# Kernel optimization log

Hardware: AMD Instinct MI355X
Metric: run time of the kernel (lower is better)

Reference implementation:

```python
import jax, jax.numpy as jnp
import numpy as np

NUM_GRAPHS = 64

def setup_inputs() -> dict:
    key = jax.random.key(0)
    ks = jax.random.split(key, 10)
    N, E, D, V = 100000, 1600000, 64, 30
    node_types = jax.random.randint(ks[0], (N,), 0, V, dtype=jnp.int64 if jax.config.jax_enable_x64 else jnp.int32)
    edge_index = jax.random.randint(ks[1], (2, E), 0, N, dtype=jnp.int32)
    batch = jnp.sort(jax.random.randint(ks[2], (N,), 0, NUM_GRAPHS, dtype=jnp.int32))
    emb_table = jax.random.normal(ks[3], (V, D), dtype=jnp.float32)
    W1 = jax.random.normal(ks[4], (D, D), dtype=jnp.float32) / np.sqrt(D)
    W2 = jax.random.normal(ks[5], (D, D), dtype=jnp.float32) / np.sqrt(D)
    W3 = jax.random.normal(ks[6], (D, D), dtype=jnp.float32) / np.sqrt(D)
    b1 = jnp.zeros((D,), jnp.float32)
    b2 = jnp.zeros((D,), jnp.float32)
    b3 = jnp.zeros((D,), jnp.float32)
    return {"node_types": node_types, "edge_index": edge_index, "batch": batch,
            "emb_table": emb_table, "W1": W1, "b1": b1, "W2": W2, "b2": b2, "W3": W3, "b3": b3}

def _gcn_conv(x, W, b, row, col, norm, N):
    # x' = D^-1/2 (A+I) D^-1/2 (x @ W) + b   (PyG GCNConv semantics)
    h = x @ W
    msg = h[row] * norm[:, None]              # gather + edgewise scale
    out = jax.ops.segment_sum(msg, col, num_segments=N)  # scatter-add at targets
    return out + b

def reference(node_types, edge_index, batch, emb_table, W1, b1, W2, b2, W3, b3):
    N = node_types.shape[0]
    # add self-loops
    loops = jnp.arange(N, dtype=edge_index.dtype)
    row = jnp.concatenate([edge_index[0], loops])
    col = jnp.concatenate([edge_index[1], loops])
    # symmetric normalization on A + I
    deg = jax.ops.segment_sum(jnp.ones_like(col, dtype=jnp.float32), col, num_segments=N)
    dinv = jnp.where(deg > 0, jax.lax.rsqrt(deg), 0.0)
    norm = dinv[row] * dinv[col]
    x = emb_table[node_types]
    x = jax.nn.relu(_gcn_conv(x, W1, b1, row, col, norm, N))
    x = jax.nn.relu(_gcn_conv(x, W2, b2, row, col, norm, N))
    x = _gcn_conv(x, W3, b3, row, col, norm, N)
    # global mean pool over batch segments
    sums = jax.ops.segment_sum(x, batch, num_segments=NUM_GRAPHS)
    cnts = jax.ops.segment_sum(jnp.ones((N,), jnp.float32), batch, num_segments=NUM_GRAPHS)
    pooled = sums / jnp.maximum(cnts, 1.0)[:, None]
    # L2 normalize rows
    return pooled / jnp.linalg.norm(pooled, axis=1, keepdims=True)
```

## Files before the change

### kernel.cpp

```cpp
#include <hip/hip_runtime.h>
#include <hip/hip_fp16.h>

#define DD 64
#define NUM_GRAPHS 64
#define AGG_BLOCKS 2048
#define EB 512
#define BINW 256
#define MAXNB 512
#define EBIN_CAP 6144

typedef _Float16 h2_t __attribute__((ext_vector_type(2)));

__device__ __forceinline__ float fdot2u(unsigned a, unsigned b, float c) {
    return __builtin_amdgcn_fdot2(__builtin_bit_cast(h2_t, a),
                                  __builtin_bit_cast(h2_t, b), c, false);
}

#define MDLO(m) __half2float(__ushort_as_half((unsigned short)((m) & 0xFFFF)))

__device__ __forceinline__ float fmixlo(float a, unsigned r) {
    float o;
    asm("v_fma_mix_f32 %0, %1, 1.0, %2 op_sel_hi:[1,0,0]"
        : "=v"(o) : "v"(r), "v"(a));
    return o;
}
__device__ __forceinline__ float fmixhi(float a, unsigned r) {
    float o;
    asm("v_fma_mix_f32 %0, %1, 1.0, %2 op_sel:[1,0,0] op_sel_hi:[1,0,0]"
        : "=v"(o) : "v"(r), "v"(a));
    return o;
}

__global__ __launch_bounds__(256) void k_hist(const int* __restrict__ col,
                                              int* __restrict__ H, int E, int NB, int CE) {
    __shared__ int h[MAXNB];
    int eb = blockIdx.x, t = threadIdx.x;
    for (int i = t; i < NB; i += 256) h[i] = 0;
    __syncthreads();
    int e0 = eb * CE, e1 = min(E, e0 + CE);
    for (int e = e0 + t; e < e1; e += 256) atomicAdd(&h[col[e] >> 8], 1);
    __syncthreads();
    for (int i = t; i < NB; i += 256) H[eb * NB + i] = h[i];
}

__global__ __launch_bounds__(256) void k_scanA(int* __restrict__ H,
                                               int* __restrict__ bintot, int NB) {
    __shared__ int s[256];
    int b = blockIdx.x, t = threadIdx.x;
    int i0 = (2 * t) * NB + b, i1 = (2 * t + 1) * NB + b;
    int v0 = H[i0], v1 = H[i1];
    int tot = v0 + v1;
    s[t] = tot;
    __syncthreads();
    for (int off = 1; off < 256; off <<= 1) {
        int tv = (t >= off) ? s[t - off] : 0;
        __syncthreads();
        s[t] += tv;
        __syncthreads();
    }
    int excl = s[t] - tot;
    H[i0] = excl;
    H[i1] = excl + v0;
    if (t == 255) bintot[b] = s[255];
}

__global__ void k_scanB(const int* __restrict__ bintot, int* __restrict__ binstart, int NB) {
    __shared__ int s[512];
    int t = threadIdx.x;
    int v = (t < NB) ? bintot[t] : 0;
    s[t] = v;
    __syncthreads();
    for (int off = 1; off < 512; off <<= 1) {
        int tv = (t >= off) ? s[t - off] : 0;
        __syncthreads();
        s[t] += tv;
        __syncthreads();
    }
    if (t < NB) binstart[t] = s[t] - v;
    if (t == 511) binstart[NB] = s[511];
}

__global__ __launch_bounds__(256) void k_scatbin(const int* __restrict__ row,
                                                 const int* __restrict__ col,
                                                 const int* __restrict__ H,
                                                 const int* __restrict__ binstart,
                                                 unsigned* __restrict__ binned,
                                                 int E, int NB, int CE) {
    __shared__ int off[MAXNB];
    int eb = blockIdx.x, t = threadIdx.x;
    for (int i = t; i < NB; i += 256) off[i] = binstart[i] + H[eb * NB + i];
    __syncthreads();
    int e0 = eb * CE, e1 = min(E, e0 + CE);
    for (int e = e0 + t; e < e1; e += 256) {
        int c = col[e], r = row[e];
        int slot = atomicAdd(&off[c >> 8], 1);
        binned[slot] = ((unsigned)(c & 255) << 24) | (unsigned)r;
    }
}

__global__ __launch_bounds__(256) void k_bincsr(const unsigned* __restrict__ binned,
                                                const int* __restrict__ binstart,
                                                const int* __restrict__ nt,
                                                int* __restrict__ srcidx,
                                                int* __restrict__ rowptr,
                                                float* __restrict__ dinv,
                                                int2* __restrict__ pk, int N, int NB) {
    __shared__ unsigned arr[EBIN_CAP];
    __shared__ int sorted_[EBIN_CAP];
    __shared__ int cnt[BINW];
    __shared__ int base[BINW];
    __shared__ int cursor[BINW];
    int b = blockIdx.x, t = threadIdx.x;
    int s0 = binstart[b], s1 = binstart[b + 1];
    int binsz = s1 - s0;
    if (binsz > EBIN_CAP) binsz = EBIN_CAP;
    cnt[t] = 0;
    for (int i = t; i < binsz; i += 256) arr[i] = binned[s0 + i];
    __syncthreads();
    for (int i = t; i < binsz; i += 256) atomicAdd(&cnt[arr[i] >> 24], 1);
    __syncthreads();
    int v = cnt[t];
    base[t] = v;
    __syncthreads();
    for (int off = 1; off < 256; off <<= 1) {
        int tv = (t >= off) ? base[t - off] : 0;
        __syncthreads();
        base[t] += tv;
        __syncthreads();
    }
    int excl = base[t] - v;
    __syncthreads();
    base[t] = excl;
    cursor[t] = excl;
    __syncthreads();
    for (int i = t; i < binsz; i += 256) {
        unsigned val = arr[i];
        int pos = atomicAdd(&cursor[val >> 24], 1);
        sorted_[pos] = (int)(val & 0xFFFFFF);
    }
    __syncthreads();
    for (int i = t; i < binsz; i += 256) srcidx[s0 + i] = sorted_[i];
    int node = b * BINW + t;
    if (node < N) {
        rowptr[node] = s0 + base[t];
        float di = rsqrtf((float)cnt[t] + 1.0f);
        dinv[node] = di;
        pk[node] = make_int2(nt[node], __float_as_int(di));
    }
    if (b == NB - 1 && t == 0) rowptr[N] = s1;
}

__global__ void k_buildepk(const int* __restrict__ srcidx, const int2* __restrict__ pk,
                           unsigned* __restrict__ epku, int E) {
    int i = blockIdx.x * blockDim.x + threadIdx.x;
    if (i >= E) return;
    int2 p = pk[srcidx[i]];
    epku[i] = ((unsigned)p.x << 16) |
              (unsigned)__half_as_ushort(__float2half(__int_as_float(p.y)));
}

__global__ void k_embW1(const float* __restrict__ emb, const float* __restrict__ W1,
                        float* __restrict__ embW1, int V) {
    __shared__ float er[DD];
    int v = blockIdx.x, j = threadIdx.x;
    er[j] = emb[v * DD + j];
    __syncthreads();
    float acc = 0.0f;
    #pragma unroll
    for (int d = 0; d < DD; ++d) acc += er[d] * W1[d * DD + j];
    embW1[v * DD + j] = acc;
}

__global__ void k_packW(const float* __restrict__ W, unsigned* __restrict__ Wpk) {
    int t = blockIdx.x * blockDim.x + threadIdx.x;
    if (t >= 32 * DD) return;
    int p = t >> 6, j = t & 63;
    __half2 h = __floats2half2_rn(W[(2 * p) * DD + j], W[(2 * p + 1) * DD + j]);
    Wpk[t] = __builtin_bit_cast(unsigned, h);
}

__device__ __forceinline__ void acc_h4(float4& a, uint2 r) {
    a.x = fmixlo(a.x, r.x); a.y = fmixhi(a.y, r.x);
    a.z = fmixlo(a.z, r.y); a.w = fmixhi(a.w, r.y);
}

__device__ __forceinline__ float4 gather_partial_q(const int* __restrict__ srcidx,
                                                   const __half* __restrict__ Hs,
                                                   int s, int e, int g, int l) {
    float4 A = {0,0,0,0}, B = {0,0,0,0}, C = {0,0,0,0}, D = {0,0,0,0};
    int k = s;
    int kend = s + ((e - s) & ~15);
    if (k < kend) {
        uint2 r0 = *(const uint2*)(Hs + (long)srcidx[k + g] * DD + 4 * l);
        uint2 r1 = *(const uint2*)(Hs + (long)srcidx[k + 4 + g] * DD + 4 * l);
        uint2 r2 = *(const uint2*)(Hs + (long)srcidx[k + 8 + g] * DD + 4 * l);
        uint2 r3 = *(const uint2*)(Hs + (long)srcidx[k + 12 + g] * DD + 4 * l);
        k += 16;
        for (; k < kend; k += 16) {
            uint2 n0 = *(const uint2*)(Hs + (long)srcidx[k + g] * DD + 4 * l);
            uint2 n1 = *(const uint2*)(Hs + (long)srcidx[k + 4 + g] * DD + 4 * l);
            uint2 n2 = *(const uint2*)(Hs + (long)srcidx[k + 8 + g] * DD + 4 * l);
            uint2 n3 = *(const uint2*)(Hs + (long)srcidx[k + 12 + g] * DD + 4 * l);
            acc_h4(A, r0); acc_h4(B, r1); acc_h4(C, r2); acc_h4(D, r3);
            r0 = n0; r1 = n1; r2 = n2; r3 = n3;
        }
        acc_h4(A, r0); acc_h4(B, r1); acc_h4(C, r2); acc_h4(D, r3);
    }
    for (; k < e; k += 4) {
        if (k + g < e) {
            uint2 rr = *(const uint2*)(Hs + (long)srcidx[k + g] * DD + 4 * l);
            acc_h4(A, rr);
        }
    }
    A.x += B.x + C.x + D.x; A.y += B.y + C.y + D.y;
    A.z += B.z + C.z + D.z; A.w += B.w + C.w + D.w;
    return A;
}

__device__ __forceinline__ void acc_h8(float4& A, float4& B, uint4 r) {
    A.x = fmixlo(A.x, r.x); A.y = fmixhi(A.y, r.x);
    A.z = fmixlo(A.z, r.y); A.w = fmixhi(A.w, r.y);
    B.x = fmixlo(B.x, r.z); B.y = fmixhi(B.y, r.z);
    B.z = fmixlo(B.z, r.w); B.w = fmixhi(B.w, r.w);
}

__device__ __forceinline__ void gather_sum_8p(const int* __restrict__ srcidx,
                                              const __half* __restrict__ Hs,
                                              int s, int e, int g, int l,
                                              float4& A, float4& B, int pi0, int pi1) {
    float4 A1 = {0.f, 0.f, 0.f, 0.f}, B1 = {0.f, 0.f, 0.f, 0.f};
    int k = s;
    int kend = s + ((e - s) & ~15);
    if (k < kend) {
        uint4 r0 = *(const uint4*)(Hs + (long)pi0 * DD + 8 * l);
        uint4 r1 = *(const uint4*)(Hs + (long)pi1 * DD + 8 * l);
        k += 16;
        for (; k < kend; k += 16) {
            uint4 n0 = *(const uint4*)(Hs + (long)srcidx[k + g] * DD + 8 * l);
            uint4 n1 = *(const uint4*)(Hs + (long)srcidx[k + 8 + g] * DD + 8 * l);
            acc_h8(A, B, r0);
            acc_h8(A1, B1, r1);
            r0 = n0; r1 = n1;
        }
        acc_h8(A, B, r0);
        acc_h8(A1, B1, r1);
    }
    if (k + 8 <= e) {
        uint4 r = *(const uint4*)(Hs + (long)srcidx[k + g] * DD + 8 * l);
        acc_h8(A, B, r);
        k += 8;
    }
    if (k + g < e) {
        uint4 r = *(const uint4*)(Hs + (long)srcidx[k + g] * DD + 8 * l);
        acc_h8(A1, B1, r);
    }
    A.x += A1.x; A.y += A1.y; A.z += A1.z; A.w += A1.w;
    B.x += B1.x; B.y += B1.y; B.z += B1.z; B.w += B1.w;
}

__global__ __launch_bounds__(256, 4) void k_agg1_fused(const int* __restrict__ rowptr,
                                                    const unsigned* __restrict__ epku,
                                                    const int2* __restrict__ pk,
                                                    const float* __restrict__ embW1,
                                                    const float* __restrict__ b1,
                                                    __half* __restrict__ OUT, int N, int V) {
    __shared__ float ew[30 * DD];
    int tid = threadIdx.x;
    for (int k = tid; k < V * DD; k += 256) ew[k] = embW1[k];
    __syncthreads();
    int lane = tid & 63;
    int g = lane >> 4, l = lane & 15;
    float4 bq = *(const float4*)(b1 + 4 * l);
    int wstride = gridDim.x * 4;
    int node = __builtin_amdgcn_readfirstlane(blockIdx.x * 4 + (tid >> 6));
    int s = 0, e = 0;
    unsigned pu0 = 0, pu1 = 0;
    if (node < N) {
        s = rowptr[node]; e = rowptr[node + 1];
        if (e - s >= 8) { pu0 = epku[s + g]; pu1 = epku[s + 4 + g]; }
    }
#define P8(U0, U1) { \
        unsigned _u0 = (U0), _u1 = (U1); \
        int _t0 = _u0 >> 16, _t1 = _u1 >> 16; \
        float _d0 = MDLO(_u0), _d1 = MDLO(_u1); \
        float4 _w0 = *(const float4*)(ew + _t0 * DD + 4 * l); \
        float4 _w1 = *(const float4*)(ew + _t1 * DD + 4 * l); \
        acc.x += _w0.x * _d0 + _w1.x * _d1; \
        acc.y += _w0.y * _d0 + _w1.y * _d1; \
        acc.z += _w0.z * _d0 + _w1.z * _d1; \
        acc.w += _w0.w * _d0 + _w1.w * _d1; }
#define P4(U0) { \
        unsigned _u0 = (U0); \
        int _t0 = _u0 >> 16; \
        float _d0 = MDLO(_u0); \
        float4 _w0 = *(const float4*)(ew + _t0 * DD + 4 * l); \
        acc.x += _w0.x * _d0; acc.y += _w0.y * _d0; \
        acc.z += _w0.z * _d0; acc.w += _w0.w * _d0; }
    while (node < N) {
        int nn = node + wstride;
        int ns = 0, ne = 0;
        if (nn < N) { ns = rowptr[nn]; ne = rowptr[nn + 1]; }
        int2 pc = pk[node];
        float4 acc = {0.f, 0.f, 0.f, 0.f};
        int k = s;
        if (k + 8 <= e) {
            P8(pu0, pu1);
            k += 8;
            for (; k + 8 <= e; k += 8) P8(epku[k + g], epku[k + 4 + g]);
        }
        if (k + 4 <= e) { P4(epku[k + g]); k += 4; }
        if (k + g < e)  { P4(epku[k + g]); }
        unsigned npu0 = 0, npu1 = 0;
        if (nn < N && ne - ns >= 8) { npu0 = epku[ns + g]; npu1 = epku[ns + 4 + g]; }
        acc.x += __shfl_xor(acc.x, 16, 64); acc.x += __shfl_xor(acc.x, 32, 64);
        acc.y += __shfl_xor(acc.y, 16, 64); acc.y += __shfl_xor(acc.y, 32, 64);
        acc.z += __shfl_xor(acc.z, 16, 64); acc.z += __shfl_xor(acc.z, 32, 64);
        acc.w += __shfl_xor(acc.w, 16, 64); acc.w += __shfl_xor(acc.w, 32, 64);
        float dc = __int_as_float(pc.y);
        float4 wc = *(const float4*)(ew + pc.x * DD + 4 * l);
        float4 v;
        v.x = fmaxf((acc.x + wc.x * dc) * dc + bq.x, 0.f) * dc;
        v.y = fmaxf((acc.y + wc.y * dc) * dc + bq.y, 0.f) * dc;
        v.z = fmaxf((acc.z + wc.z * dc) * dc + bq.z, 0.f) * dc;
        v.w = fmaxf((acc.w + wc.w * dc) * dc + bq.w, 0.f) * dc;
        if (g == 0) {
            __half2 h0 = __floats2half2_rn(v.x, v.y);
            __half2 h1 = __floats2half2_rn(v.z, v.w);
            uint2 st;
            st.x = __builtin_bit_cast(unsigned, h0);
            st.y = __builtin_bit_cast(unsigned, h1);
            *(uint2*)(OUT + (long)node * DD + 4 * l) = st;
        }
        node = nn; s = ns; e = ne; pu0 = npu0; pu1 = npu1;
    }
#undef P8
#undef P4
}

__global__ __launch_bounds__(256, 4) void k_agg2_fused(const int* __restrict__ rowptr,
                                                    const int* __restrict__ srcidx,
                                                    const float* __restrict__ dinv,
                                                    const __half* __restrict__ Hs,
                                                    const float* __restrict__ b2,
                                                    const unsigned* __restrict__ W2pk,
                                                    __half* __restrict__ OUT, int N) {
    int tid = threadIdx.x;
    int lane = tid & 63;
    int g = lane >> 3, l = lane & 7;
    unsigned Wc[32];
    #pragma unroll
    for (int p = 0; p < 32; ++p) Wc[p] = W2pk[p * DD + lane];
    float bl = b2[lane];
    int wstride = gridDim.x * 4;
    int node = __builtin_amdgcn_readfirstlane(blockIdx.x * 4 + (tid >> 6));
    int s = 0, e = 0;
    int pi0 = 0, pi1 = 0;
    if (node < N) {
        s = rowptr[node]; e = rowptr[node + 1];
        if (e - s >= 16) { pi0 = srcidx[s + g]; pi1 = srcidx[s + 8 + g]; }
    }
    while (node < N) {
        int nn = node + wstride;
        int ns = 0, ne = 0;
        if (nn < N) { ns = rowptr[nn]; ne = rowptr[nn + 1]; }
        float dc = dinv[node];
        uint4 sr = *(const uint4*)(Hs + (long)node * DD + 8 * l);
        float4 A = {0.f, 0.f, 0.f, 0.f}, B = {0.f, 0.f, 0.f, 0.f};
        gather_sum_8p(srcidx, Hs, s, e, g, l, A, B, pi0, pi1);
        int npi0 = 0, npi1 = 0;
        if (nn < N && ne - ns >= 16) { npi0 = srcidx[ns + g]; npi1 = srcidx[ns + 8 + g]; }
        #pragma unroll
        for (int m = 8; m <= 32; m <<= 1) {
            A.x += __shfl_xor(A.x, m, 64); A.y += __shfl_xor(A.y, m, 64);
            A.z += __shfl_xor(A.z, m, 64); A.w += __shfl_xor(A.w, m, 64);
            B.x += __shfl_xor(B.x, m, 64); B.y += __shfl_xor(B.y, m, 64);
            B.z += __shfl_xor(B.z, m, 64); B.w += __shfl_xor(B.w, m, 64);
        }
        float2 s0 = __half22float2(*(const __half2*)&sr.x);
        float2 s1 = __half22float2(*(const __half2*)&sr.y);
        float2 s2 = __half22float2(*(const __half2*)&sr.z);
        float2 s3 = __half22float2(*(const __half2*)&sr.w);
        float t0 = (A.x + s0.x) * dc, t1 = (A.y + s0.y) * dc;
        float t2 = (A.z + s1.x) * dc, t3 = (A.w + s1.y) * dc;
        float t4 = (B.x + s2.x) * dc, t5 = (B.y + s2.y) * dc;
        float t6 = (B.z + s3.x) * dc, t7 = (B.w + s3.y) * dc;
        int vp0 = __builtin_bit_cast(int, __floats2half2_rn(t0, t1));
        int vp1 = __builtin_bit_cast(int, __floats2half2_rn(t2, t3));
        int vp2 = __builtin_bit_cast(int, __floats2half2_rn(t4, t5));
        int vp3 = __builtin_bit_cast(int, __floats2half2_rn(t6, t7));
        float o0 = 0.f, o1 = 0.f, o2 = 0.f, o3 = 0.f;
        #pragma unroll
        for (int p = 0; p < 32; p += 4) {
            o0 = fdot2u((unsigned)__builtin_amdgcn_readlane(vp0, p >> 2), Wc[p + 0], o0);
            o1 = fdot2u((unsigned)__builtin_amdgcn_readlane(vp1, p >> 2), Wc[p + 1], o1);
            o2 = fdot2u((unsigned)__builtin_amdgcn_readlane(vp2, p >> 2), Wc[p + 2], o2);
            o3 = fdot2u((unsigned)__builtin_amdgcn_readlane(vp3, p >> 2), Wc[p + 3], o3);
        }
        float u = (o0 + o1) + (o2 + o3);
        float v2 = fmaxf(u + bl, 0.f);
        OUT[(long)node * DD + lane] = __float2half(v2 * dc);
        node = nn; s = ns; e = ne; pi0 = npi0; pi1 = npi1;
    }
}

__device__ __forceinline__ void flush_pool_q(float4& PA, float* __restrict__ pool,
                                             int gcur, int g, int l) {
    gcur &= (NUM_GRAPHS - 1);
    PA.x += __shfl_xor(PA.x, 16, 64); PA.x += __shfl_xor(PA.x, 32, 64);
    PA.y += __shfl_xor(PA.y, 16, 64); PA.y += __shfl_xor(PA.y, 32, 64);
    PA.z += __shfl_xor(PA.z, 16, 64); PA.z += __shfl_xor(PA.z, 32, 64);
    PA.w += __shfl_xor(PA.w, 16, 64); PA.w += __shfl_xor(PA.w, 32, 64);
    if (g == 0) {
        atomicAdd(&pool[gcur * DD + 4 * l + 0], PA.x);
        atomicAdd(&pool[gcur * DD + 4 * l + 1], PA.y);
        atomicAdd(&pool[gcur * DD + 4 * l + 2], PA.z);
        atomicAdd(&pool[gcur * DD + 4 * l + 3], PA.w);
    }
}

__global__ __launch_bounds__(256, 4) void k_agg3_pool(const int* __restrict__ rowptr,
                                                   const int* __restrict__ srcidx,
                                                   const float* __restrict__ dinv,
                                                   const __half* __restrict__ Hs,
                                                   const int* __restrict__ batch,
                                                   float* __restrict__ pool,
                                                   int N, int chunk) {
    int tid = threadIdx.x;
    int lane = tid & 63;
    int g = lane >> 4, l = lane & 15;
    int w = __builtin_amdgcn_readfirstlane(blockIdx.x * 4 + (tid >> 6));
    int start = w * chunk;
    if (start >= N) return;
    int endn = min(N, start + chunk);
    int gcur = batch[start];
    float4 PA = {0.f, 0.f, 0.f, 0.f};
    int s = rowptr[start];
    for (int node = start; node < endn; ++node) {
        int e = rowptr[node + 1];
        float dc = dinv[node];
        int gb = batch[node];
        uint2 sr = *(const uint2*)(Hs + (long)node * DD + 4 * l);
        float4 A = gather_partial_q(srcidx, Hs, s, e, g, l);
        if (g == 0) {
            A.x = fmixlo(A.x, sr.x); A.y = fmixhi(A.y, sr.x);
            A.z = fmixlo(A.z, sr.y); A.w = fmixhi(A.w, sr.y);
        }
        if (gb != gcur) {
            flush_pool_q(PA, pool, gcur, g, l);
            gcur = gb;
            PA.x = dc * A.x; PA.y = dc * A.y; PA.z = dc * A.z; PA.w = dc * A.w;
        } else {
            PA.x += dc * A.x; PA.y += dc * A.y; PA.z += dc * A.z; PA.w += dc * A.w;
        }
        s = e;
    }
    flush_pool_q(PA, pool, gcur, g, l);
}

__global__ void k_final(const float* __restrict__ pool, const int* __restrict__ batch,
                        const float* __restrict__ W3, const float* __restrict__ b3,
                        float* __restrict__ out, int N) {
    __shared__ float pr[DD];
    int g = blockIdx.x, j = threadIdx.x;
    pr[j] = pool[g * DD + j];
    __syncthreads();
    int lo = 0, hi = N;
    while (lo < hi) { int m = (lo + hi) >> 1; if (batch[m] < g) lo = m + 1; else hi = m; }
    int lo2 = lo; hi = N;
    while (lo2 < hi) { int m = (lo2 + hi) >> 1; if (batch[m] < g + 1) lo2 = m + 1; else hi = m; }
    float cnt = fmaxf((float)(lo2 - lo), 1.0f);
    float acc = 0.0f;
    #pragma unroll
    for (int d = 0; d < DD; ++d) acc += pr[d] * W3[d * DD + j];
    float v = acc / cnt + b3[j];
    float sq = v * v;
    #pragma unroll
    for (int off = 32; off > 0; off >>= 1) sq += __shfl_down(sq, off, 64);
    float nrm = __shfl(sq, 0, 64);
    out[g * DD + j] = v / sqrtf(nrm);
}

extern "C" void kernel_launch(void* const* d_in, const int* in_sizes, int n_in,
                              void* d_out, int out_size, void* d_ws, size_t ws_size,
                              hipStream_t stream) {
    const int*   node_types = (const int*)d_in[0];
    const int*   edge_index = (const int*)d_in[1];
    const int*   batch      = (const int*)d_in[2];
    const float* emb        = (const float*)d_in[3];
    const float* W1 = (const float*)d_in[4];
    const float* b1 = (const float*)d_in[5];
    const float* W2 = (const float*)d_in[6];
    const float* b2 = (const float*)d_in[7];
    const float* W3 = (const float*)d_in[8];
    const float* b3 = (const float*)d_in[9];
    const int N = in_sizes[0];
    const int E = in_sizes[1] / 2;
    const int V = in_sizes[3] / DD;
    const int* row = edge_index;
    const int* col = edge_index + E;
    const long ND = (long)N * DD;
    const int NB = (N + BINW - 1) / BINW;
    const int CE = (E + EB - 1) / EB;

    char* p = (char*)d_ws;
    __half*   hsA     = (__half*)p;       p += ND * sizeof(__half);
    __half*   hsB     = (__half*)p;       p += ND * sizeof(__half);
    int*      srcidx  = (int*)p;          p += (size_t)E * sizeof(int);
    unsigned* epku    = (unsigned*)p;     p += (size_t)E * sizeof(unsigned);
    unsigned* binned  = (unsigned*)p;     p += (size_t)E * sizeof(unsigned);
    int*      H       = (int*)p;          p += (size_t)EB * NB * sizeof(int);
    int*      bintot  = (int*)p;          p += (size_t)(NB + 4) * sizeof(int);
    int*      binstart= (int*)p;          p += (size_t)(NB + 4) * sizeof(int);
    float*    dinv    = (float*)p;        p += (size_t)N * sizeof(float);
    int2*     pk      = (int2*)p;         p += (size_t)N * sizeof(int2);
    int*      rowptr  = (int*)p;          p += (size_t)(N + 4) * sizeof(int);
    float*    pool    = (float*)p;        p += (size_t)NUM_GRAPHS * DD * sizeof(float);
    float*    embW1   = (float*)p;        p += (size_t)V * DD * sizeof(float);
    unsigned* W2pk    = (unsigned*)p;     p += 32 * DD * sizeof(unsigned);

    k_hist<<<EB, 256, 0, stream>>>(col, H, E, NB, CE);
    k_scanA<<<NB, 256, 0, stream>>>(H, bintot, NB);
    k_scanB<<<1, 512, 0, stream>>>(bintot, binstart, NB);
    k_scatbin<<<EB, 256, 0, stream>>>(row, col, H, binstart, binned, E, NB, CE);
    k_bincsr<<<NB, 256, 0, stream>>>(binned, binstart, node_types, srcidx, rowptr,
                                     dinv, pk, N, NB);
    k_buildepk<<<(E + 255) / 256, 256, 0, stream>>>(srcidx, pk, epku, E);

    k_embW1<<<V, DD, 0, stream>>>(emb, W1, embW1, V);
    k_packW<<<8, 256, 0, stream>>>(W2, W2pk);

    k_agg1_fused<<<AGG_BLOCKS, 256, 0, stream>>>(rowptr, epku, pk, embW1, b1,
                                                 hsA, N, V);
    k_agg2_fused<<<AGG_BLOCKS, 256, 0, stream>>>(rowptr, srcidx, dinv, hsA, b2, W2pk,
                                                 hsB, N);
    hipMemsetAsync(pool, 0, (size_t)(NUM_GRAPHS * DD) * sizeof(float), stream);
    const int totalWaves = AGG_BLOCKS * 4;
    const int chunk = (N + totalWaves - 1) / totalWaves;
    k_agg3_pool<<<AGG_BLOCKS, 256, 0, stream>>>(rowptr, srcidx, dinv, hsB, batch,
                                                pool, N, chunk);
    k_final<<<NUM_GRAPHS, DD, 0, stream>>>(pool, batch, W3, b3, (float*)d_out, N);
}
```

Measured before the change: 272.0 us.

## Split layer-3 pooling into edge-balanced gather and separate self-loop pass

The final layer's aggregate-and-pool kernel now partitions work by equal edge ranges per wave instead of node ranges. Each edge carries a packed word holding the target's graph id and its fp16 dinv, so the kernel can scale and pool straight into per-graph accumulators. The packed word is built in the CSR build kernel and written into the reused binned buffer. Self-loop contributions move to a new small kernel. This is meant to remove load imbalance and per-node rowptr/dinv/batch lookups, at the cost of an extra launch, extra writes in bincsr, and fp16 rounding of dinv.

New measurement: 351.5 us. 29.2% more time.

```diff
diff --git a/kernel.cpp b/kernel.cpp
--- a/kernel.cpp
+++ b/kernel.cpp
@@ -8,6 +8,7 @@
 #define BINW 256
 #define MAXNB 512
 #define EBIN_CAP 6144
+#define EPAD 512
 
 typedef _Float16 h2_t __attribute__((ext_vector_type(2)));
 
@@ -28,6 +29,18 @@
     float o;
     asm("v_fma_mix_f32 %0, %1, 1.0, %2 op_sel:[1,0,0] op_sel_hi:[1,0,0]"
         : "=v"(o) : "v"(r), "v"(a));
+    return o;
+}
+__device__ __forceinline__ float fmixlo_m(float a, unsigned r, float m) {
+    float o;
+    asm("v_fma_mix_f32 %0, %1, %2, %3 op_sel_hi:[1,0,0]"
+        : "=v"(o) : "v"(r), "v"(m), "v"(a));
+    return o;
+}
+__device__ __forceinline__ float fmixhi_m(float a, unsigned r, float m) {
+    float o;
+    asm("v_fma_mix_f32 %0, %1, %2, %3 op_sel:[1,0,0] op_sel_hi:[1,0,0]"
+        : "=v"(o) : "v"(r), "v"(m), "v"(a));
     return o;
 }
 
@@ -98,18 +111,21 @@
     }
 }
 
-__global__ __launch_bounds__(256) void k_bincsr(const unsigned* __restrict__ binned,
+__global__ __launch_bounds__(256) void k_bincsr(const unsigned* binned,
                                                 const int* __restrict__ binstart,
                                                 const int* __restrict__ nt,
+                                                const int* __restrict__ batch,
                                                 int* __restrict__ srcidx,
                                                 int* __restrict__ rowptr,
                                                 float* __restrict__ dinv,
-                                                int2* __restrict__ pk, int N, int NB) {
+                                                int2* __restrict__ pk,
+                                                unsigned* e3pk, int N, int NB) {
     __shared__ unsigned arr[EBIN_CAP];
     __shared__ int sorted_[EBIN_CAP];
     __shared__ int cnt[BINW];
     __shared__ int base[BINW];
     __shared__ int cursor[BINW];
+    __shared__ unsigned packS[BINW];
     int b = blockIdx.x, t = threadIdx.x;
     int s0 = binstart[b], s1 = binstart[b + 1];
     int binsz = s1 - s0;
@@ -120,6 +136,13 @@
     for (int i = t; i < binsz; i += 256) atomicAdd(&cnt[arr[i] >> 24], 1);
     __syncthreads();
     int v = cnt[t];
+    float di = rsqrtf((float)v + 1.0f);
+    {
+        int nodeT = b * BINW + t;
+        int bt = (nodeT < N) ? batch[nodeT] : 0;
+        packS[t] = ((unsigned)bt << 16) |
+                   (unsigned)__half_as_ushort(__float2half(di));
+    }
     base[t] = v;
     __syncthreads();
     for (int off = 1; off < 256; off <<= 1) {
@@ -135,15 +158,16 @@
     __syncthreads();
     for (int i = t; i < binsz; i += 256) {
         unsigned val = arr[i];
-        int pos = atomicAdd(&cursor[val >> 24], 1);
+        int d = val >> 24;
+        int pos = atomicAdd(&cursor[d], 1);
         sorted_[pos] = (int)(val & 0xFFFFFF);
+        e3pk[s0 + pos] = packS[d];
     }
     __syncthreads();
     for (int i = t; i < binsz; i += 256) srcidx[s0 + i] = sorted_[i];
     int node = b * BINW + t;
     if (node < N) {
         rowptr[node] = s0 + base[t];
-        float di = rsqrtf((float)cnt[t] + 1.0f);
         dinv[node] = di;
         pk[node] = make_int2(nt[node], __float_as_int(di));
     }
@@ -177,44 +201,6 @@
     int p = t >> 6, j = t & 63;
     __half2 h = __floats2half2_rn(W[(2 * p) * DD + j], W[(2 * p + 1) * DD + j]);
     Wpk[t] = __builtin_bit_cast(unsigned, h);
-}
-
-__device__ __forceinline__ void acc_h4(float4& a, uint2 r) {
-    a.x = fmixlo(a.x, r.x); a.y = fmixhi(a.y, r.x);
-    a.z = fmixlo(a.z, r.y); a.w = fmixhi(a.w, r.y);
-}
-
-__device__ __forceinline__ float4 gather_partial_q(const int* __restrict__ srcidx,
-                                                   const __half* __restrict__ Hs,
-                                                   int s, int e, int g, int l) {
-    float4 A = {0,0,0,0}, B = {0,0,0,0}, C = {0,0,0,0}, D = {0,0,0,0};
-    int k = s;
-    int kend = s + ((e - s) & ~15);
-    if (k < kend) {
-        uint2 r0 = *(const uint2*)(Hs + (long)srcidx[k + g] * DD + 4 * l);
-        uint2 r1 = *(const uint2*)(Hs + (long)srcidx[k + 4 + g] * DD + 4 * l);
-        uint2 r2 = *(const uint2*)(Hs + (long)srcidx[k + 8 + g] * DD + 4 * l);
-        uint2 r3 = *(const uint2*)(Hs + (long)srcidx[k + 12 + g] * DD + 4 * l);
-        k += 16;
-        for (; k < kend; k += 16) {
-            uint2 n0 = *(const uint2*)(Hs + (long)srcidx[k + g] * DD + 4 * l);
-            uint2 n1 = *(const uint2*)(Hs + (long)srcidx[k + 4 + g] * DD + 4 * l);
-            uint2 n2 = *(const uint2*)(Hs + (long)srcidx[k + 8 + g] * DD + 4 * l);
-            uint2 n3 = *(const uint2*)(Hs + (long)srcidx[k + 12 + g] * DD + 4 * l);
-            acc_h4(A, r0); acc_h4(B, r1); acc_h4(C, r2); acc_h4(D, r3);
-            r0 = n0; r1 = n1; r2 = n2; r3 = n3;
-        }
-        acc_h4(A, r0); acc_h4(B, r1); acc_h4(C, r2); acc_h4(D, r3);
-    }
-    for (; k < e; k += 4) {
-        if (k + g < e) {
-            uint2 rr = *(const uint2*)(Hs + (long)srcidx[k + g] * DD + 4 * l);
-            acc_h4(A, rr);
-        }
-    }
-    A.x += B.x + C.x + D.x; A.y += B.y + C.y + D.y;
-    A.z += B.z + C.z + D.z; A.w += B.w + C.w + D.w;
-    return A;
 }
 
 __device__ __forceinline__ void acc_h8(float4& A, float4& B, uint4 r) {
@@ -418,43 +404,102 @@
     }
 }
 
-__global__ __launch_bounds__(256, 4) void k_agg3_pool(const int* __restrict__ rowptr,
-                                                   const int* __restrict__ srcidx,
-                                                   const float* __restrict__ dinv,
+__global__ __launch_bounds__(256, 4) void k_agg3_pool(const int* __restrict__ srcidx,
+                                                   const unsigned* __restrict__ e3pk,
                                                    const __half* __restrict__ Hs,
-                                                   const int* __restrict__ batch,
                                                    float* __restrict__ pool,
-                                                   int N, int chunk) {
+                                                   int E, int ech) {
     int tid = threadIdx.x;
     int lane = tid & 63;
     int g = lane >> 4, l = lane & 15;
+    int w = __builtin_amdgcn_readfirstlane(blockIdx.x * 4 + (tid >> 6));
+    int k0 = w * ech;
+    if (k0 >= E) return;
+    int kend = k0 + ech;
+    int gA = (int)(e3pk[k0] >> 16);
+    float4 accA = {0.f, 0.f, 0.f, 0.f}, accB = {0.f, 0.f, 0.f, 0.f};
+    unsigned m0 = e3pk[k0 + g],      m1 = e3pk[k0 + 4 + g];
+    unsigned m2 = e3pk[k0 + 8 + g],  m3 = e3pk[k0 + 12 + g];
+    int s0 = srcidx[k0 + g],         s1 = srcidx[k0 + 4 + g];
+    int s2 = srcidx[k0 + 8 + g],     s3 = srcidx[k0 + 12 + g];
+    uint2 r0 = *(const uint2*)(Hs + (long)s0 * DD + 4 * l);
+    uint2 r1 = *(const uint2*)(Hs + (long)s1 * DD + 4 * l);
+    uint2 r2 = *(const uint2*)(Hs + (long)s2 * DD + 4 * l);
+    uint2 r3 = *(const uint2*)(Hs + (long)s3 * DD + 4 * l);
+    for (int k = k0; k < kend; k += 16) {
+        int kn = k + 16;
+        unsigned nm0 = e3pk[kn + g],      nm1 = e3pk[kn + 4 + g];
+        unsigned nm2 = e3pk[kn + 8 + g],  nm3 = e3pk[kn + 12 + g];
+        int ns0 = srcidx[kn + g],         ns1 = srcidx[kn + 4 + g];
+        int ns2 = srcidx[kn + 8 + g],     ns3 = srcidx[kn + 12 + g];
+        uint2 nr0 = *(const uint2*)(Hs + (long)ns0 * DD + 4 * l);
+        uint2 nr1 = *(const uint2*)(Hs + (long)ns1 * DD + 4 * l);
+        uint2 nr2 = *(const uint2*)(Hs + (long)ns2 * DD + 4 * l);
+        uint2 nr3 = *(const uint2*)(Hs + (long)ns3 * DD + 4 * l);
+        int bF = __builtin_amdgcn_readfirstlane((int)(m0 >> 16));
+        int bL = __builtin_amdgcn_readlane((int)(m3 >> 16), 48);
+        int target = min(bF, NUM_GRAPHS - 1);
+        while (gA < target) {
+            flush_pool_q(accA, pool, gA, g, l);
+            accA = accB;
+            accB.x = 0.f; accB.y = 0.f; accB.z = 0.f; accB.w = 0.f;
+            ++gA;
+        }
+        if (bF == gA && bL == gA) {
+            float d0 = MDLO(m0), d1 = MDLO(m1), d2 = MDLO(m2), d3 = MDLO(m3);
+            accA.x = fmixlo_m(accA.x, r0.x, d0); accA.y = fmixhi_m(accA.y, r0.x, d0);
+            accA.z = fmixlo_m(accA.z, r0.y, d0); accA.w = fmixhi_m(accA.w, r0.y, d0);
+            accA.x = fmixlo_m(accA.x, r1.x, d1); accA.y = fmixhi_m(accA.y, r1.x, d1);
+            accA.z = fmixlo_m(accA.z, r1.y, d1); accA.w = fmixhi_m(accA.w, r1.y, d1);
+            accA.x = fmixlo_m(accA.x, r2.x, d2); accA.y = fmixhi_m(accA.y, r2.x, d2);
+            accA.z = fmixlo_m(accA.z, r2.y, d2); accA.w = fmixhi_m(accA.w, r2.y, d2);
+            accA.x = fmixlo_m(accA.x, r3.x, d3); accA.y = fmixhi_m(accA.y, r3.x, d3);
+            accA.z = fmixlo_m(accA.z, r3.y, d3); accA.w = fmixhi_m(accA.w, r3.y, d3);
+        } else {
+            #define EDGE_P(M, R) { \
+                int _b = (int)((M) >> 16); \
+                float _d = MDLO(M); \
+                float _dA = (_b == gA)     ? _d : 0.f; \
+                float _dB = (_b == gA + 1) ? _d : 0.f; \
+                accA.x = fmixlo_m(accA.x, (R).x, _dA); accA.y = fmixhi_m(accA.y, (R).x, _dA); \
+                accA.z = fmixlo_m(accA.z, (R).y, _dA); accA.w = fmixhi_m(accA.w, (R).y, _dA); \
+                accB.x = fmixlo_m(accB.x, (R).x, _dB); accB.y = fmixhi_m(accB.y, (R).x, _dB); \
+                accB.z = fmixlo_m(accB.z, (R).y, _dB); accB.w = fmixhi_m(accB.w, (R).y, _dB); }
+            EDGE_P(m0, r0); EDGE_P(m1, r1); EDGE_P(m2, r2); EDGE_P(m3, r3);
+            #undef EDGE_P
+        }
+        m0 = nm0; m1 = nm1; m2 = nm2; m3 = nm3;
+        r0 = nr0; r1 = nr1; r2 = nr2; r3 = nr3;
+    }
+    flush_pool_q(accA, pool, gA, g, l);
+    flush_pool_q(accB, pool, gA + 1, g, l);
+}
+
+__global__ __launch_bounds__(256, 4) void k_self3(const float* __restrict__ dinv,
+                                               const __half* __restrict__ Hs,
+                                               const int* __restrict__ batch,
+                                               float* __restrict__ pool,
+                                               int N, int chunk) {
+    int tid = threadIdx.x;
+    int lane = tid & 63;
     int w = __builtin_amdgcn_readfirstlane(blockIdx.x * 4 + (tid >> 6));
     int start = w * chunk;
     if (start >= N) return;
     int endn = min(N, start + chunk);
     int gcur = batch[start];
-    float4 PA = {0.f, 0.f, 0.f, 0.f};
-    int s = rowptr[start];
-    for (int node = start; node < endn; ++node) {
-        int e = rowptr[node + 1];
-        float dc = dinv[node];
-        int gb = batch[node];
-        uint2 sr = *(const uint2*)(Hs + (long)node * DD + 4 * l);
-        float4 A = gather_partial_q(srcidx, Hs, s, e, g, l);
-        if (g == 0) {
-            A.x = fmixlo(A.x, sr.x); A.y = fmixhi(A.y, sr.x);
-            A.z = fmixlo(A.z, sr.y); A.w = fmixhi(A.w, sr.y);
-        }
+    float acc = 0.f;
+    for (int n = start; n < endn; ++n) {
+        int gb = batch[n];
+        float v = __half2float(Hs[(long)n * DD + lane]);
+        float dc = dinv[n];
         if (gb != gcur) {
-            flush_pool_q(PA, pool, gcur, g, l);
+            atomicAdd(&pool[gcur * DD + lane], acc);
+            acc = 0.f;
             gcur = gb;
-            PA.x = dc * A.x; PA.y = dc * A.y; PA.z = dc * A.z; PA.w = dc * A.w;
-        } else {
-            PA.x += dc * A.x; PA.y += dc * A.y; PA.z += dc * A.z; PA.w += dc * A.w;
-        }
-        s = e;
-    }
-    flush_pool_q(PA, pool, gcur, g, l);
+        }
+        acc += dc * v;
+    }
+    atomicAdd(&pool[gcur * DD + lane], acc);
 }
 
 __global__ void k_final(const float* __restrict__ pool, const int* __restrict__ batch,
@@ -505,9 +550,9 @@
     char* p = (char*)d_ws;
     __half*   hsA     = (__half*)p;       p += ND * sizeof(__half);
     __half*   hsB     = (__half*)p;       p += ND * sizeof(__half);
-    int*      srcidx  = (int*)p;          p += (size_t)E * sizeof(int);
+    int*      srcidx  = (int*)p;          p += (size_t)(E + EPAD) * sizeof(int);
     unsigned* epku    = (unsigned*)p;     p += (size_t)E * sizeof(unsigned);
-    unsigned* binned  = (unsigned*)p;     p += (size_t)E * sizeof(unsigned);
+    unsigned* binned  = (unsigned*)p;     p += (size_t)(E + EPAD) * sizeof(unsigned);
     int*      H       = (int*)p;          p += (size_t)EB * NB * sizeof(int);
     int*      bintot  = (int*)p;          p += (size_t)(NB + 4) * sizeof(int);
     int*      binstart= (int*)p;          p += (size_t)(NB + 4) * sizeof(int);
@@ -517,13 +562,17 @@
     float*    pool    = (float*)p;        p += (size_t)NUM_GRAPHS * DD * sizeof(float);
     float*    embW1   = (float*)p;        p += (size_t)V * DD * sizeof(float);
     unsigned* W2pk    = (unsigned*)p;     p += 32 * DD * sizeof(unsigned);
+    unsigned* e3pk    = binned;
+
+    hipMemsetAsync(srcidx + E, 0, EPAD * sizeof(int), stream);
+    hipMemsetAsync(e3pk + E, 0xFF, EPAD * sizeof(unsigned), stream);
 
     k_hist<<<EB, 256, 0, stream>>>(col, H, E, NB, CE);
     k_scanA<<<NB, 256, 0, stream>>>(H, bintot, NB);
     k_scanB<<<1, 512, 0, stream>>>(bintot, binstart, NB);
     k_scatbin<<<EB, 256, 0, stream>>>(row, col, H, binstart, binned, E, NB, CE);
-    k_bincsr<<<NB, 256, 0, stream>>>(binned, binstart, node_types, srcidx, rowptr,
-                                     dinv, pk, N, NB);
+    k_bincsr<<<NB, 256, 0, stream>>>(binned, binstart, node_types, batch, srcidx,
+                                     rowptr, dinv, pk, e3pk, N, NB);
     k_buildepk<<<(E + 255) / 256, 256, 0, stream>>>(srcidx, pk, epku, E);
 
     k_embW1<<<V, DD, 0, stream>>>(emb, W1, embW1, V);
@@ -535,8 +584,9 @@
                                                  hsB, N);
     hipMemsetAsync(pool, 0, (size_t)(NUM_GRAPHS * DD) * sizeof(float), stream);
     const int totalWaves = AGG_BLOCKS * 4;
-    const int chunk = (N + totalWaves - 1) / totalWaves;
-    k_agg3_pool<<<AGG_BLOCKS, 256, 0, stream>>>(rowptr, srcidx, dinv, hsB, batch,
-                                                pool, N, chunk);
+    const int ech = (((E + totalWaves - 1) / totalWaves) + 15) & ~15;
+    k_agg3_pool<<<AGG_BLOCKS, 256, 0, stream>>>(srcidx, e3pk, hsB, pool, E, ech);
+    const int chunkN = (N + totalWaves - 1) / totalWaves;
+    k_self3<<<AGG_BLOCKS, 256, 0, stream>>>(dinv, hsB, batch, pool, N, chunkN);
     k_final<<<NUM_GRAPHS, DD, 0, stream>>>(pool, batch, W3, b3, (float*)d_out, N);
 }
```
